# Performance work log

Hardware: AMD Instinct MI355X
Metric: run time of the kernel (lower is better)

## Reference

```python
import jax, jax.numpy as jnp
import numpy as np

N, C, H, W = 8, 256, 31, 31
HIDDEN, OUT = 512, 256


def setup_inputs() -> dict:
    key = jax.random.key(0)
    k0, k1, k2, k3, k4 = jax.random.split(key, 5)
    x = jax.random.normal(k0, (N, C, H, W), dtype=jnp.float32)
    # Linear params (torch nn.Linear layout: [out_features, in_features])
    W1 = jax.random.normal(k1, (HIDDEN, C), dtype=jnp.float32) * (1.0 / np.sqrt(C))
    b1 = jax.random.normal(k2, (HIDDEN,), dtype=jnp.float32) * 0.01
    W2 = jax.random.normal(k3, (OUT, HIDDEN), dtype=jnp.float32) * (1.0 / np.sqrt(HIDDEN))
    b2 = jax.random.normal(k4, (OUT,), dtype=jnp.float32) * 0.01
    return {"x": x, "W1": W1, "b1": b1, "W2": W2, "b2": b2}


def _normalized_adjacency(n, h, w):
    M = n * h * w
    idx = jnp.arange(M)
    blk = idx // (h * w)          # sample id of each node
    pos = idx % (h * w)           # spatial position within sample
    # block-diagonal all-ones per sample
    same_block = (blk[:, None] == blk[None, :]).astype(jnp.float32)
    # identity link between consecutive samples (disjoint from block-diag)
    neighbor = ((jnp.abs(blk[:, None] - blk[None, :]) == 1)
                & (pos[:, None] == pos[None, :])).astype(jnp.float32)
    A = same_block + neighbor + jnp.eye(M, dtype=jnp.float32)
    deg = A.sum(axis=1)
    dinv = jnp.where(deg > 0, deg ** -0.5, 0.0)
    return A * dinv[:, None] * dinv[None, :]  # D^-1/2 A D^-1/2


def reference(x, W1, b1, W2, b2):
    n, c, h, w = x.shape
    weight = _normalized_adjacency(n, h, w)                 # [M, M]
    nodes = x.transpose(0, 2, 3, 1).reshape(-1, c)          # [M, C]
    hid = jax.nn.leaky_relu(weight @ nodes @ W1.T + b1)     # [M, HIDDEN]
    hid = jax.nn.leaky_relu(weight @ hid @ W2.T + b2)       # [M, OUT]
    hid = hid.reshape(n, h, w, -1).transpose(0, 3, 1, 2)    # [N, OUT, H, W]
    return hid.max(axis=0, keepdims=True)                   # [1, OUT, H, W]
```

## Files before the change

### kernel.cpp

```cpp
#include <hip/hip_runtime.h>
#include <math.h>

#define NS   8
#define CC   256
#define PP   961
#define MM   7688
#define MP   7744
#define HID  512
#define OUTC 256

typedef _Float16 h16;
using half8   = __attribute__((ext_vector_type(8))) _Float16;
using floatx4 = __attribute__((ext_vector_type(4))) float;

#define AS1 __attribute__((address_space(1)))
#define AS3 __attribute__((address_space(3)))

__device__ __forceinline__ float dinv_of(int b) {
    return (b == 0 || b == NS - 1) ? 0.0322245515f : 0.0322078318f;
}

__global__ void prep(const float* __restrict__ W1, const float* __restrict__ W2,
                     h16* __restrict__ w1h, h16* __restrict__ w2h,
                     const float* __restrict__ x, float* __restrict__ S1,
                     float* __restrict__ SY) {
    int blk = blockIdx.x, tid = threadIdx.x;
    if (blk < 256) {
        bool second = blk >= 128;
        const float* src = second ? W2 : W1;
        h16* dst = second ? w2h : w1h;
        int i = ((blk & 127) * 256 + tid) * 4;
        float4 v = *(const float4*)(src + i);
        dst[i + 0] = (h16)v.x; dst[i + 1] = (h16)v.y;
        dst[i + 2] = (h16)v.z; dst[i + 3] = (h16)v.w;
    } else if (blk < 2304) {
        int bc = blk - 256;
        const float* src = x + (size_t)bc * PP;
        float s = 0.f;
        for (int i = tid; i < PP; i += 256) s += src[i];
        __shared__ float red[256];
        red[tid] = s;
        __syncthreads();
        for (int off = 128; off > 0; off >>= 1) {
            if (tid < off) red[tid] += red[tid + off];
            __syncthreads();
        }
        if (tid == 0) S1[bc] = red[0];
    } else {
        int i = (blk - 2304) * 256 + tid;
        SY[i] = 0.f;
    }
}

__global__ void build_g1(const float* __restrict__ x, const float* __restrict__ S1,
                         h16* __restrict__ G1) {
    int pt = blockIdx.x, ct = blockIdx.y, b = blockIdx.z;
    int p0 = pt * 32, c0 = ct * 32;
    float db  = dinv_of(b);
    float wm  = (b > 0)      ? db * dinv_of(b - 1) : 0.f;
    float wp  = (b < NS - 1) ? db * dinv_of(b + 1) : 0.f;
    float db2 = db * db;
    __shared__ float t[32][33];
    int j = threadIdx.x & 31, i0 = threadIdx.x >> 5;
    int p = p0 + j;
    bool pv = (p < PP);
    #pragma unroll
    for (int r = 0; r < 4; ++r) {
        int i = i0 + r * 8;
        int c = c0 + i;
        float v = 0.f;
        if (pv) {
            size_t base = ((size_t)b * CC + c) * PP + p;
            float xb = x[base];
            float xm = (b > 0)      ? x[base - (size_t)CC * PP] : 0.f;
            float xp = (b < NS - 1) ? x[base + (size_t)CC * PP] : 0.f;
            v = db2 * (S1[b * CC + c] + xb) + wm * xm + wp * xp;
        }
        t[i][j] = v;
    }
    __syncthreads();
    int ii = threadIdx.x & 31, jj0 = threadIdx.x >> 5;
    #pragma unroll
    for (int r = 0; r < 4; ++r) {
        int jj = jj0 + r * 8;
        int pw = p0 + jj;
        if (pw < PP)
            G1[((size_t)b * PP + pw) * CC + c0 + ii] = (h16)t[ii][jj];
    }
}

template<int KD, bool ACT, bool DO_SUM, typename OutT>
__global__ __launch_bounds__(256) void mfma_gemm(
    const h16* __restrict__ A,
    const h16* __restrict__ B,
    const float* __restrict__ bias,
    OutT* __restrict__ C,
    float* __restrict__ SY,
    int M, int Nc)
{
    __shared__ __align__(16) h16 As[64 * 64];
    __shared__ __align__(16) h16 Bs[64 * 64];
    int tid = threadIdx.x, wave = tid >> 6, lane = tid & 63;
    int m0 = blockIdx.x * 64, n0 = blockIdx.y * 64;
    int sro = lane >> 3;
    int sch = (lane & 7) ^ sro;
    const h16* ga0 = A + (size_t)(m0 + wave * 16 + sro) * KD + sch * 8;
    const h16* gb0 = B + (size_t)(n0 + wave * 16 + sro) * KD + sch * 8;
    h16* la0 = &As[(wave * 16) * 64];
    h16* la1 = &As[(wave * 16 + 8) * 64];
    h16* lb0 = &Bs[(wave * 16) * 64];
    h16* lb1 = &Bs[(wave * 16 + 8) * 64];
    int fr = lane & 15, fq = lane >> 4;
    floatx4 acc[4] = {{0.f,0.f,0.f,0.f},{0.f,0.f,0.f,0.f},{0.f,0.f,0.f,0.f},{0.f,0.f,0.f,0.f}};
    for (int kk = 0; kk < KD; kk += 64) {
        __builtin_amdgcn_global_load_lds((const AS1 void*)(const void*)(ga0 + kk),
                                         (AS3 void*)(void*)la0, 16, 0, 0);
        __builtin_amdgcn_global_load_lds((const AS1 void*)(const void*)(ga0 + 8 * KD + kk),
                                         (AS3 void*)(void*)la1, 16, 0, 0);
        __builtin_amdgcn_global_load_lds((const AS1 void*)(const void*)(gb0 + kk),
                                         (AS3 void*)(void*)lb0, 16, 0, 0);
        __builtin_amdgcn_global_load_lds((const AS1 void*)(const void*)(gb0 + 8 * KD + kk),
                                         (AS3 void*)(void*)lb1, 16, 0, 0);
        __syncthreads();
        #pragma unroll
        for (int ks = 0; ks < 2; ++ks) {
            int slot = (ks * 4 + fq) ^ (fr & 7);
            half8 bf = *(const half8*)&Bs[(wave * 16 + fr) * 64 + slot * 8];
            #pragma unroll
            for (int mb = 0; mb < 4; ++mb) {
                half8 af = *(const half8*)&As[(mb * 16 + fr) * 64 + slot * 8];
                acc[mb] = __builtin_amdgcn_mfma_f32_16x16x32_f16(af, bf, acc[mb], 0, 0, 0);
            }
        }
        __syncthreads();
    }
    int col = n0 + wave * 16 + fr;
    float bv = ACT ? bias[col] : 0.f;
    float s_lo = 0.f, s_hi = 0.f;
    int blo = m0 / 961;
    int mcut = (blo + 1) * 961;
    #pragma unroll
    for (int mb = 0; mb < 4; ++mb) {
        #pragma unroll
        for (int r = 0; r < 4; ++r) {
            int m = m0 + mb * 16 + fq * 4 + r;
            if (m < M) {
                float v = acc[mb][r] + bv;
                if (ACT) v = (v >= 0.f) ? v : 0.01f * v;
                C[(size_t)m * Nc + col] = (OutT)v;
                if (DO_SUM) { if (m < mcut) s_lo += v; else s_hi += v; }
            }
        }
    }
    if (DO_SUM) {
        s_lo += __shfl_xor(s_lo, 16);
        s_lo += __shfl_xor(s_lo, 32);
        s_hi += __shfl_xor(s_hi, 16);
        s_hi += __shfl_xor(s_hi, 32);
        if (fq == 0) {
            atomicAdd(&SY[blo * Nc + col], s_lo);
            int bhi = (m0 + 63) / 961;
            if (bhi != blo && bhi < NS) atomicAdd(&SY[bhi * Nc + col], s_hi);
        }
    }
}

__global__ void final_max(const float* __restrict__ Y, const float* __restrict__ SY,
                          const float* __restrict__ b2, float* __restrict__ out) {
    int pt = blockIdx.x, ot = blockIdx.y;
    int p0 = pt * 32, o0 = ot * 32;
    __shared__ float t[32][33];
    int i = threadIdx.x & 31, j0 = threadIdx.x >> 5;
    int o = o0 + i;
    float bias = b2[o];
    #pragma unroll
    for (int r = 0; r < 4; ++r) {
        int j = j0 + r * 8;
        int p = p0 + j;
        float vmax = -INFINITY;
        if (p < PP) {
            float y[NS];
            #pragma unroll
            for (int b = 0; b < NS; ++b)
                y[b] = Y[((size_t)b * PP + p) * OUTC + o];
            #pragma unroll
            for (int b = 0; b < NS; ++b) {
                float db = dinv_of(b);
                float a = db * (SY[b * OUTC + o] + y[b]);
                if (b > 0)      a += dinv_of(b - 1) * y[b - 1];
                if (b < NS - 1) a += dinv_of(b + 1) * y[b + 1];
                float z = db * a + bias;
                z = (z >= 0.f) ? z : 0.01f * z;
                vmax = fmaxf(vmax, z);
            }
        }
        t[j][i] = vmax;
    }
    __syncthreads();
    int jj = threadIdx.x & 31, ii0 = threadIdx.x >> 5;
    #pragma unroll
    for (int r = 0; r < 4; ++r) {
        int ii = ii0 + r * 8;
        int pw = p0 + jj;
        if (pw < PP)
            out[(size_t)(o0 + ii) * PP + pw] = t[jj][ii];
    }
}

extern "C" void kernel_launch(void* const* d_in, const int* in_sizes, int n_in,
                              void* d_out, int out_size, void* d_ws, size_t ws_size,
                              hipStream_t stream) {
    const float* x  = (const float*)d_in[0];
    const float* W1 = (const float*)d_in[1];
    const float* b1 = (const float*)d_in[2];
    const float* W2 = (const float*)d_in[3];
    const float* b2 = (const float*)d_in[4];
    float* out = (float*)d_out;
    float* ws  = (float*)d_ws;

    float* S1  = ws;
    float* SY  = ws + 2048;
    h16*  w1h  = (h16*)(ws + 4096);
    h16*  w2h  = (h16*)(ws + 69632);
    h16*  G1   = (h16*)(ws + 135168);
    h16*  H1   = (h16*)(ws + 1126400);
    float* Y   = ws + 3108864;

    prep<<<2312, 256, 0, stream>>>(W1, W2, w1h, w2h, x, S1, SY);
    build_g1<<<dim3(31, 8, NS), 256, 0, stream>>>(x, S1, G1);
    mfma_gemm<CC, true, false, h16><<<dim3(MP / 64, HID / 64), 256, 0, stream>>>(
        G1, w1h, b1, H1, nullptr, MM, HID);
    mfma_gemm<HID, false, true, float><<<dim3(MP / 64, OUTC / 64), 256, 0, stream>>>(
        H1, w2h, nullptr, Y, SY, MM, OUTC);
    final_max<<<dim3(31, 8), 256, 0, stream>>>(Y, SY, b2, out);
}
```

Baseline: 95.41 us.

## Reorder layer-1 to GEMM-first and fuse adjacency aggregation into second GEMM prologue

Layer 1 now runs x·W1ᵀ first, on a plain half-precision transpose of x, and collects per-sample column sums of the result with atomics. The adjacency aggregation, bias and leaky-relu are then applied while building the A tile inside the second GEMM. That tile is read from three row-shifted views of Z (current, previous and next sample). This removes the separate build_g1 kernel and the full G1/H1 round-trip, at the cost of three times the A-tile loads in GEMM2. It also adds an extra shared-memory pass and a sync per k-step. Summing the fp16-stored Z values could change numerics slightly.

Measured after the change: 101.6 us. +6.5%, slower.

```diff
diff --git a/kernel.cpp b/kernel.cpp
--- a/kernel.cpp
+++ b/kernel.cpp
@@ -22,8 +22,8 @@
 
 __global__ void prep(const float* __restrict__ W1, const float* __restrict__ W2,
                      h16* __restrict__ w1h, h16* __restrict__ w2h,
-                     const float* __restrict__ x, float* __restrict__ S1,
-                     float* __restrict__ SY) {
+                     const float* __restrict__ x, h16* __restrict__ Xt,
+                     float* __restrict__ SZ, float* __restrict__ SY) {
     int blk = blockIdx.x, tid = threadIdx.x;
     if (blk < 256) {
         bool second = blk >= 128;
@@ -33,59 +33,32 @@
         float4 v = *(const float4*)(src + i);
         dst[i + 0] = (h16)v.x; dst[i + 1] = (h16)v.y;
         dst[i + 2] = (h16)v.z; dst[i + 3] = (h16)v.w;
-    } else if (blk < 2304) {
-        int bc = blk - 256;
-        const float* src = x + (size_t)bc * PP;
-        float s = 0.f;
-        for (int i = tid; i < PP; i += 256) s += src[i];
-        __shared__ float red[256];
-        red[tid] = s;
-        __syncthreads();
-        for (int off = 128; off > 0; off >>= 1) {
-            if (tid < off) red[tid] += red[tid + off];
-            __syncthreads();
-        }
-        if (tid == 0) S1[bc] = red[0];
+    } else if (blk < 2240) {
+        __shared__ h16 tr[32][33];
+        int t = blk - 256;
+        int b = t & 7, ct = (t >> 3) & 7, pt = t >> 6;
+        int p0 = pt * 32, c0 = ct * 32;
+        int j = tid & 31, i0 = tid >> 5;
+        int p = p0 + j;
+        #pragma unroll
+        for (int r = 0; r < 4; ++r) {
+            int c = c0 + i0 + r * 8;
+            float v = (p < PP) ? x[((size_t)b * CC + c) * PP + p] : 0.f;
+            tr[i0 + r * 8][j] = (h16)v;
+        }
+        __syncthreads();
+        #pragma unroll
+        for (int r = 0; r < 4; ++r) {
+            int ii = tid & 31;
+            int jj = (tid >> 5) + r * 8;
+            int pw = p0 + jj;
+            if (pw < PP)
+                Xt[((size_t)b * PP + pw) * CC + c0 + ii] = tr[ii][jj];
+        }
     } else {
-        int i = (blk - 2304) * 256 + tid;
-        SY[i] = 0.f;
-    }
-}
-
-__global__ void build_g1(const float* __restrict__ x, const float* __restrict__ S1,
-                         h16* __restrict__ G1) {
-    int pt = blockIdx.x, ct = blockIdx.y, b = blockIdx.z;
-    int p0 = pt * 32, c0 = ct * 32;
-    float db  = dinv_of(b);
-    float wm  = (b > 0)      ? db * dinv_of(b - 1) : 0.f;
-    float wp  = (b < NS - 1) ? db * dinv_of(b + 1) : 0.f;
-    float db2 = db * db;
-    __shared__ float t[32][33];
-    int j = threadIdx.x & 31, i0 = threadIdx.x >> 5;
-    int p = p0 + j;
-    bool pv = (p < PP);
-    #pragma unroll
-    for (int r = 0; r < 4; ++r) {
-        int i = i0 + r * 8;
-        int c = c0 + i;
-        float v = 0.f;
-        if (pv) {
-            size_t base = ((size_t)b * CC + c) * PP + p;
-            float xb = x[base];
-            float xm = (b > 0)      ? x[base - (size_t)CC * PP] : 0.f;
-            float xp = (b < NS - 1) ? x[base + (size_t)CC * PP] : 0.f;
-            v = db2 * (S1[b * CC + c] + xb) + wm * xm + wp * xp;
-        }
-        t[i][j] = v;
-    }
-    __syncthreads();
-    int ii = threadIdx.x & 31, jj0 = threadIdx.x >> 5;
-    #pragma unroll
-    for (int r = 0; r < 4; ++r) {
-        int jj = jj0 + r * 8;
-        int pw = p0 + jj;
-        if (pw < PP)
-            G1[((size_t)b * PP + pw) * CC + c0 + ii] = (h16)t[ii][jj];
+        int i = (blk - 2240) * 256 + tid;
+        if (i < NS * HID) SZ[i] = 0.f;
+        else SY[i - NS * HID] = 0.f;
     }
 }
 
@@ -95,7 +68,7 @@
     const h16* __restrict__ B,
     const float* __restrict__ bias,
     OutT* __restrict__ C,
-    float* __restrict__ SY,
+    float* __restrict__ S,
     int M, int Nc)
 {
     __shared__ __align__(16) h16 As[64 * 64];
@@ -158,10 +131,128 @@
         s_hi += __shfl_xor(s_hi, 16);
         s_hi += __shfl_xor(s_hi, 32);
         if (fq == 0) {
-            atomicAdd(&SY[blo * Nc + col], s_lo);
+            atomicAdd(&S[blo * Nc + col], s_lo);
             int bhi = (m0 + 63) / 961;
-            if (bhi != blo && bhi < NS) atomicAdd(&SY[bhi * Nc + col], s_hi);
-        }
+            if (bhi != blo && bhi < NS) atomicAdd(&S[bhi * Nc + col], s_hi);
+        }
+    }
+}
+
+__global__ __launch_bounds__(256) void gemm2_fused(
+    const h16* __restrict__ Z,
+    const h16* __restrict__ B,
+    const float* __restrict__ SZ,
+    const float* __restrict__ b1v,
+    float* __restrict__ C,
+    float* __restrict__ SY)
+{
+    __shared__ __align__(16) h16 Zc[64 * 64];
+    __shared__ __align__(16) h16 Zm[64 * 64];
+    __shared__ __align__(16) h16 Zp[64 * 64];
+    __shared__ __align__(16) h16 Hs[64 * 64];
+    __shared__ __align__(16) h16 Bs[64 * 64];
+    int tid = threadIdx.x, wave = tid >> 6, lane = tid & 63;
+    int m0 = blockIdx.x * 64, n0 = blockIdx.y * 64;
+    int sro = lane >> 3;
+    int sch = (lane & 7) ^ sro;
+    const h16* gzc = Z + (ptrdiff_t)(m0 + wave * 16 + sro) * HID + sch * 8;
+    const h16* gzm = gzc - (ptrdiff_t)PP * HID;
+    const h16* gzp = gzc + (ptrdiff_t)PP * HID;
+    const h16* gbb = B + (size_t)(n0 + wave * 16 + sro) * HID + sch * 8;
+    h16* lzc0 = &Zc[(wave * 16) * 64];     h16* lzc1 = &Zc[(wave * 16 + 8) * 64];
+    h16* lzm0 = &Zm[(wave * 16) * 64];     h16* lzm1 = &Zm[(wave * 16 + 8) * 64];
+    h16* lzp0 = &Zp[(wave * 16) * 64];     h16* lzp1 = &Zp[(wave * 16 + 8) * 64];
+    h16* lb0  = &Bs[(wave * 16) * 64];     h16* lb1  = &Bs[(wave * 16 + 8) * 64];
+    int fr = lane & 15, fq = lane >> 4;
+    int hr = tid >> 2;
+    int hc0 = (tid & 3) * 2;
+    int hm = m0 + hr;
+    int hb = hm / PP; if (hb > NS - 1) hb = NS - 1;
+    float db = dinv_of(hb);
+    float dm = (hb > 0)      ? db * dinv_of(hb - 1) : 0.f;
+    float dp = (hb < NS - 1) ? db * dinv_of(hb + 1) : 0.f;
+    float db2 = db * db;
+    floatx4 acc[4] = {{0.f,0.f,0.f,0.f},{0.f,0.f,0.f,0.f},{0.f,0.f,0.f,0.f},{0.f,0.f,0.f,0.f}};
+    for (int kk = 0; kk < HID; kk += 64) {
+        __builtin_amdgcn_global_load_lds((const AS1 void*)(const void*)(gzc + kk),
+                                         (AS3 void*)(void*)lzc0, 16, 0, 0);
+        __builtin_amdgcn_global_load_lds((const AS1 void*)(const void*)(gzc + 8 * HID + kk),
+                                         (AS3 void*)(void*)lzc1, 16, 0, 0);
+        __builtin_amdgcn_global_load_lds((const AS1 void*)(const void*)(gzm + kk),
+                                         (AS3 void*)(void*)lzm0, 16, 0, 0);
+        __builtin_amdgcn_global_load_lds((const AS1 void*)(const void*)(gzm + 8 * HID + kk),
+                                         (AS3 void*)(void*)lzm1, 16, 0, 0);
+        __builtin_amdgcn_global_load_lds((const AS1 void*)(const void*)(gzp + kk),
+                                         (AS3 void*)(void*)lzp0, 16, 0, 0);
+        __builtin_amdgcn_global_load_lds((const AS1 void*)(const void*)(gzp + 8 * HID + kk),
+                                         (AS3 void*)(void*)lzp1, 16, 0, 0);
+        __builtin_amdgcn_global_load_lds((const AS1 void*)(const void*)(gbb + kk),
+                                         (AS3 void*)(void*)lb0, 16, 0, 0);
+        __builtin_amdgcn_global_load_lds((const AS1 void*)(const void*)(gbb + 8 * HID + kk),
+                                         (AS3 void*)(void*)lb1, 16, 0, 0);
+        __syncthreads();
+        #pragma unroll
+        for (int qi = 0; qi < 2; ++qi) {
+            int ch = hc0 + qi;
+            int slot = ch ^ (hr & 7);
+            int off = hr * 64 + slot * 8;
+            half8 zc = *(const half8*)&Zc[off];
+            half8 zm = *(const half8*)&Zm[off];
+            half8 zp = *(const half8*)&Zp[off];
+            int h0 = kk + ch * 8;
+            float4 s0  = *(const float4*)(SZ + hb * HID + h0);
+            float4 s1  = *(const float4*)(SZ + hb * HID + h0 + 4);
+            float4 bb0 = *(const float4*)(b1v + h0);
+            float4 bb1 = *(const float4*)(b1v + h0 + 4);
+            float ss[8] = {s0.x, s0.y, s0.z, s0.w, s1.x, s1.y, s1.z, s1.w};
+            float bb[8] = {bb0.x, bb0.y, bb0.z, bb0.w, bb1.x, bb1.y, bb1.z, bb1.w};
+            half8 o;
+            #pragma unroll
+            for (int j = 0; j < 8; ++j) {
+                float v = db2 * (ss[j] + (float)zc[j])
+                        + dm * (float)zm[j] + dp * (float)zp[j] + bb[j];
+                v = (v >= 0.f) ? v : 0.01f * v;
+                o[j] = (h16)v;
+            }
+            *(half8*)&Hs[off] = o;
+        }
+        __syncthreads();
+        #pragma unroll
+        for (int ks = 0; ks < 2; ++ks) {
+            int slot = (ks * 4 + fq) ^ (fr & 7);
+            half8 bf = *(const half8*)&Bs[(wave * 16 + fr) * 64 + slot * 8];
+            #pragma unroll
+            for (int mb = 0; mb < 4; ++mb) {
+                half8 af = *(const half8*)&Hs[(mb * 16 + fr) * 64 + slot * 8];
+                acc[mb] = __builtin_amdgcn_mfma_f32_16x16x32_f16(af, bf, acc[mb], 0, 0, 0);
+            }
+        }
+        __syncthreads();
+    }
+    int col = n0 + wave * 16 + fr;
+    float s_lo = 0.f, s_hi = 0.f;
+    int blo = m0 / 961;
+    int mcut = (blo + 1) * 961;
+    #pragma unroll
+    for (int mb = 0; mb < 4; ++mb) {
+        #pragma unroll
+        for (int r = 0; r < 4; ++r) {
+            int m = m0 + mb * 16 + fq * 4 + r;
+            if (m < MM) {
+                float v = acc[mb][r];
+                C[(size_t)m * OUTC + col] = v;
+                if (m < mcut) s_lo += v; else s_hi += v;
+            }
+        }
+    }
+    s_lo += __shfl_xor(s_lo, 16);
+    s_lo += __shfl_xor(s_lo, 32);
+    s_hi += __shfl_xor(s_hi, 16);
+    s_hi += __shfl_xor(s_hi, 32);
+    if (fq == 0) {
+        atomicAdd(&SY[blo * OUTC + col], s_lo);
+        int bhi = (m0 + 63) / 961;
+        if (bhi != blo && bhi < NS) atomicAdd(&SY[bhi * OUTC + col], s_hi);
     }
 }
 
@@ -218,19 +309,18 @@
     float* out = (float*)d_out;
     float* ws  = (float*)d_ws;
 
-    float* S1  = ws;
-    float* SY  = ws + 2048;
-    h16*  w1h  = (h16*)(ws + 4096);
-    h16*  w2h  = (h16*)(ws + 69632);
-    h16*  G1   = (h16*)(ws + 135168);
-    h16*  H1   = (h16*)(ws + 1126400);
-    float* Y   = ws + 3108864;
-
-    prep<<<2312, 256, 0, stream>>>(W1, W2, w1h, w2h, x, S1, SY);
-    build_g1<<<dim3(31, 8, NS), 256, 0, stream>>>(x, S1, G1);
-    mfma_gemm<CC, true, false, h16><<<dim3(MP / 64, HID / 64), 256, 0, stream>>>(
-        G1, w1h, b1, H1, nullptr, MM, HID);
-    mfma_gemm<HID, false, true, float><<<dim3(MP / 64, OUTC / 64), 256, 0, stream>>>(
-        H1, w2h, nullptr, Y, SY, MM, OUTC);
+    float* SZ  = ws;
+    float* SY  = ws + 4096;
+    h16*  w1h  = (h16*)(ws + 6144);
+    h16*  w2h  = (h16*)(ws + 71680);
+    h16*  Xt   = (h16*)(ws + 137216);
+    h16*  Zbuf = (h16*)(ws + 1128448);
+    h16*  Z    = Zbuf + (size_t)1024 * HID;
+    float* Y   = ws + 3635200;
+
+    prep<<<2264, 256, 0, stream>>>(W1, W2, w1h, w2h, x, Xt, SZ, SY);
+    mfma_gemm<CC, false, true, h16><<<dim3(MP / 64, HID / 64), 256, 0, stream>>>(
+        Xt, w1h, nullptr, Z, SZ, MM, HID);
+    gemm2_fused<<<dim3(MP / 64, OUTC / 64), 256, 0, stream>>>(Z, w2h, SZ, b1, Y, SY);
     final_max<<<dim3(31, 8), 256, 0, stream>>>(Y, SY, b2, out);
 }
```
